# Kernel tuning notes

Measured on AMD Instinct MI355X. Metric: run time of the kernel, lower is better.

## Reference

```python
import jax, jax.numpy as jnp
import numpy as np

B, S, D, H, L, F = 16, 256, 512, 1024, 2, 2048  # batch, seq, inner, head(clusters), layers, ffnn
HID = D // 2
LN_EPS = 1e-5


def _lstm_dir(x, Wih, Whh, bih, bhh, reverse=False):
    # x: [B,S,D] -> hs: [B,S,HID]; PyTorch gate order i,f,g,o
    if reverse:
        x = x[:, ::-1]
    xT = jnp.swapaxes(x, 0, 1)                    # [S,B,D]
    pre = xT @ Wih.T + (bih + bhh)                # precompute input contribution [S,B,4*HID]
    z = jnp.zeros((x.shape[0], Whh.shape[1]), x.dtype)

    def step(carry, p):
        h, c = carry
        g = p + h @ Whh.T
        i, f, gg, o = jnp.split(g, 4, axis=-1)
        c = jax.nn.sigmoid(f) * c + jax.nn.sigmoid(i) * jnp.tanh(gg)
        h = jax.nn.sigmoid(o) * jnp.tanh(c)
        return (h, c), h

    _, hs = jax.lax.scan(step, (z, z), pre)
    hs = jnp.swapaxes(hs, 0, 1)                   # [B,S,HID]
    if reverse:
        hs = hs[:, ::-1]
    return hs


def _layernorm(x, g, b):
    mu = jnp.mean(x, axis=-1, keepdims=True)
    var = jnp.mean(jnp.square(x - mu), axis=-1, keepdims=True)
    return (x - mu) * jax.lax.rsqrt(var + LN_EPS) * g + b


def _forward(input_sequence, label_embeddings, out_proj,
             Wih_f, Whh_f, bih_f, bhh_f, Wih_b, Whh_b, bih_b, bhh_b,
             ffnn_w1, ffnn_b1, ffnn_w2, ffnn_b2, ln_g, ln_b):
    fwd = _lstm_dir(input_sequence, Wih_f, Whh_f, bih_f, bhh_f, reverse=False)
    bwd = _lstm_dir(input_sequence, Wih_b, Whh_b, bih_b, bhh_b, reverse=True)
    features = jnp.concatenate([fwd, bwd], axis=-1)          # [B,S,D]

    query = jnp.broadcast_to(label_embeddings, (input_sequence.shape[0], H, D))
    for l in range(L):
        # self-attention (no scaling, as in source)
        w = jax.nn.softmax(jnp.einsum('bqd,bkd->bqk', query, query), axis=-1)
        q1 = jnp.einsum('bqk,bkd->bqd', w, query)
        # cross-attention onto LSTM features
        w2 = jax.nn.softmax(jnp.einsum('bqd,bsd->bqs', q1, features), axis=-1)
        q2 = jnp.einsum('bqs,bsd->bqd', w2, features)
        # FFN + LayerNorm
        h = jax.nn.gelu(q2 @ ffnn_w1[l] + ffnn_b1[l], approximate=False) @ ffnn_w2[l] + ffnn_b2[l]
        query = _layernorm(h, ln_g[l], ln_b[l])
    # (query @ output) * eye @ ones  ==  diagonal of the matmul == batched dot
    return jnp.einsum('bhd,dh->bh', query, out_proj)


def setup_inputs() -> dict:
    ks = jax.random.split(jax.random.key(0), 20)
    s_lstm = 1.0 / np.sqrt(HID)
    s_ff = 0.02
    clusters = jax.random.normal(ks[0], (H, D), jnp.float32) * s_ff
    return {
        'input_sequence': jax.random.normal(ks[1], (B, S, D), jnp.float32),
        'label_embeddings': clusters,
        'out_proj': clusters.T,
        'Wih_f': jax.random.normal(ks[2], (4 * HID, D), jnp.float32) * s_lstm,
        'Whh_f': jax.random.normal(ks[3], (4 * HID, HID), jnp.float32) * s_lstm,
        'bih_f': jax.random.normal(ks[4], (4 * HID,), jnp.float32) * s_lstm,
        'bhh_f': jax.random.normal(ks[5], (4 * HID,), jnp.float32) * s_lstm,
        'Wih_b': jax.random.normal(ks[6], (4 * HID, D), jnp.float32) * s_lstm,
        'Whh_b': jax.random.normal(ks[7], (4 * HID, HID), jnp.float32) * s_lstm,
        'bih_b': jax.random.normal(ks[8], (4 * HID,), jnp.float32) * s_lstm,
        'bhh_b': jax.random.normal(ks[9], (4 * HID,), jnp.float32) * s_lstm,
        'ffnn_w1': jax.random.normal(ks[10], (L, D, F), jnp.float32) * s_ff,
        'ffnn_b1': jnp.zeros((L, F), jnp.float32),
        'ffnn_w2': jax.random.normal(ks[11], (L, F, D), jnp.float32) * s_ff,
        'ffnn_b2': jnp.zeros((L, D), jnp.float32),
        'ln_g': jnp.ones((L, D), jnp.float32),
        'ln_b': jnp.zeros((L, D), jnp.float32),
    }


def reference(input_sequence, label_embeddings, out_proj,
              Wih_f, Whh_f, bih_f, bhh_f, Wih_b, Whh_b, bih_b, bhh_b,
              ffnn_w1, ffnn_b1, ffnn_w2, ffnn_b2, ln_g, ln_b):
    return _forward(input_sequence, label_embeddings, out_proj,
                    Wih_f, Whh_f, bih_f, bhh_f, Wih_b, Whh_b, bih_b, bhh_b,
                    ffnn_w1, ffnn_b1, ffnn_w2, ffnn_b2, ln_g, ln_b)
```

## Files before the change

kernel.cpp:

```cpp
#include <hip/hip_runtime.h>
#include <hip/hip_bf16.h>
#include <math.h>

#define NB 16
#define NS 256
#define ND 512
#define NH 1024
#define NF 2048
#define NHID 256

typedef __attribute__((ext_vector_type(8))) short bf16x8;
typedef __attribute__((ext_vector_type(4))) float f32x4;

__device__ __forceinline__ unsigned short f2bf(float f) {
    unsigned u = __float_as_uint(f);
    unsigned r = u + 0x7fffu + ((u >> 16) & 1u);
    return (unsigned short)(r >> 16);
}
__device__ __forceinline__ float bf2f(unsigned short h) {
    return __uint_as_float(((unsigned)h) << 16);
}
__device__ __forceinline__ float sigmoid_fast(float x) {
    return 1.0f / (1.0f + __expf(-x));
}
__device__ __forceinline__ float tanh_fast(float x) {
    return 1.0f - 2.0f / (__expf(2.0f * x) + 1.0f);
}

template<int PASSES, int ACT, int OUT>
__global__ __launch_bounds__(256) void sgemm4(
    const unsigned short* __restrict__ Ahi, const unsigned short* __restrict__ Alo,
    const unsigned short* __restrict__ Bhi, const unsigned short* __restrict__ Blo,
    const float* __restrict__ bias,
    float* __restrict__ C, unsigned short* __restrict__ Chi, unsigned short* __restrict__ Clo,
    int M, int N, int K, int lda, int ldb, long sA, long sB, long sC)
{
    __shared__ unsigned short Ah[128 * 32];
    __shared__ unsigned short Bh[128 * 32];
    __shared__ unsigned short Al[(PASSES == 3) ? 128 * 32 : 64];
    __shared__ unsigned short Bl[(PASSES == 3) ? 128 * 32 : 64];

    const int t = threadIdx.x;
    const int z = blockIdx.z;
    const int m0 = blockIdx.y * 128, n0 = blockIdx.x * 128;
    const int wid = t >> 6, lane = t & 63;
    const int wr = (wid >> 1) * 64, wc = (wid & 1) * 64;
    const int lr = lane & 15, lk = lane >> 4;
    const int rl = lane >> 2, sl = lane & 3;

    const unsigned short* pAh = Ahi + (size_t)z * sA;
    const unsigned short* pBh = Bhi + (size_t)z * sB;
    const unsigned short* pAl = (PASSES == 3) ? Alo + (size_t)z * sA : nullptr;
    const unsigned short* pBl = (PASSES == 3) ? Blo + (size_t)z * sB : nullptr;

    f32x4 acc[4][4];
    #pragma unroll
    for (int i = 0; i < 4; ++i)
        #pragma unroll
        for (int j = 0; j < 4; ++j) acc[i][j] = (f32x4){0.f, 0.f, 0.f, 0.f};

    for (int k0 = 0; k0 < K; k0 += 32) {
        #pragma unroll
        for (int e = 0; e < 2; ++e) {
            const int r = e * 64 + wid * 16 + rl;
            const size_t goA = (size_t)(m0 + r) * lda + k0 + sl * 8;
            const size_t goB = (size_t)(n0 + r) * ldb + k0 + sl * 8;
            const int lo = (e * 64 + wid * 16) * 32;
            __builtin_amdgcn_global_load_lds((const void*)(pAh + goA), (void*)&Ah[lo], 16, 0, 0);
            __builtin_amdgcn_global_load_lds((const void*)(pBh + goB), (void*)&Bh[lo], 16, 0, 0);
            if (PASSES == 3) {
                __builtin_amdgcn_global_load_lds((const void*)(pAl + goA), (void*)&Al[lo], 16, 0, 0);
                __builtin_amdgcn_global_load_lds((const void*)(pBl + goB), (void*)&Bl[lo], 16, 0, 0);
            }
        }
        __syncthreads();

        bf16x8 ah[4], bh[4], al[4], bl[4];
        #pragma unroll
        for (int mt = 0; mt < 4; ++mt) {
            int rf = wr + mt * 16 + lr;
            ah[mt] = *(const bf16x8*)&Ah[rf * 32 + lk * 8];
            if (PASSES == 3) al[mt] = *(const bf16x8*)&Al[rf * 32 + lk * 8];
        }
        #pragma unroll
        for (int nt = 0; nt < 4; ++nt) {
            int rf = wc + nt * 16 + lr;
            bh[nt] = *(const bf16x8*)&Bh[rf * 32 + lk * 8];
            if (PASSES == 3) bl[nt] = *(const bf16x8*)&Bl[rf * 32 + lk * 8];
        }
        #pragma unroll
        for (int mt = 0; mt < 4; ++mt)
            #pragma unroll
            for (int nt = 0; nt < 4; ++nt) {
                acc[mt][nt] = __builtin_amdgcn_mfma_f32_16x16x32_bf16(ah[mt], bh[nt], acc[mt][nt], 0, 0, 0);
                if (PASSES == 3) {
                    acc[mt][nt] = __builtin_amdgcn_mfma_f32_16x16x32_bf16(al[mt], bh[nt], acc[mt][nt], 0, 0, 0);
                    acc[mt][nt] = __builtin_amdgcn_mfma_f32_16x16x32_bf16(ah[mt], bl[nt], acc[mt][nt], 0, 0, 0);
                }
            }
        __syncthreads();
    }

    #pragma unroll
    for (int nt = 0; nt < 4; ++nt) {
        int col = n0 + wc + nt * 16 + lr;
        float bv = bias ? bias[col] : 0.0f;
        #pragma unroll
        for (int mt = 0; mt < 4; ++mt) {
            #pragma unroll
            for (int i = 0; i < 4; ++i) {
                int row = m0 + wr + mt * 16 + lk * 4 + i;
                float x = acc[mt][nt][i] + bv;
                if (ACT == 1) x = 0.5f * x * (1.0f + erff(x * 0.70710678118654752f));
                size_t oi = (size_t)z * sC + (size_t)row * N + col;
                if (OUT == 1) {
                    unsigned short h = f2bf(x);
                    Chi[oi] = h;
                    Clo[oi] = f2bf(x - bf2f(h));
                } else if (OUT == 2) {
                    Chi[oi] = f2bf(x);
                } else {
                    C[oi] = x;
                }
            }
        }
    }
}

static void gemm4(int passes, int act, int outm,
                  const unsigned short* Ahi, const unsigned short* Alo,
                  const unsigned short* Bhi, const unsigned short* Blo,
                  const float* bias, float* C, unsigned short* Chi, unsigned short* Clo,
                  int M, int N, int K, int lda, int ldb,
                  long sA, long sB, long sC, int Z, hipStream_t st)
{
    dim3 g(N / 128, M / 128, Z), b(256);
    if (passes == 3) {
        sgemm4<3, 0, 0><<<g, b, 0, st>>>(Ahi, Alo, Bhi, Blo, bias, C, Chi, Clo, M, N, K, lda, ldb, sA, sB, sC);
    } else if (outm == 1) {
        sgemm4<1, 0, 1><<<g, b, 0, st>>>(Ahi, Alo, Bhi, Blo, bias, C, Chi, Clo, M, N, K, lda, ldb, sA, sB, sC);
    } else if (outm == 2 && act == 1) {
        sgemm4<1, 1, 2><<<g, b, 0, st>>>(Ahi, Alo, Bhi, Blo, bias, C, Chi, Clo, M, N, K, lda, ldb, sA, sB, sC);
    } else if (outm == 2) {
        sgemm4<1, 0, 2><<<g, b, 0, st>>>(Ahi, Alo, Bhi, Blo, bias, C, Chi, Clo, M, N, K, lda, ldb, sA, sB, sC);
    } else {
        sgemm4<1, 0, 0><<<g, b, 0, st>>>(Ahi, Alo, Bhi, Blo, bias, C, Chi, Clo, M, N, K, lda, ldb, sA, sB, sC);
    }
}

__global__ __launch_bounds__(256) void ffn2_ln(
    const unsigned short* __restrict__ A, const unsigned short* __restrict__ B,
    const float* __restrict__ bias, const float* __restrict__ g, const float* __restrict__ bb,
    unsigned short* __restrict__ Ohi, unsigned short* __restrict__ Olo)
{
    __shared__ unsigned short Ah[64 * 32];
    __shared__ unsigned short Bh[512 * 32];
    __shared__ float stats[64][4][2];

    const int t = threadIdx.x;
    const int m0 = blockIdx.x * 64;
    const int wid = t >> 6, lane = t & 63;
    const int lr = lane & 15, lk = lane >> 4;
    const int wc = wid * 128;
    const int rl = lane >> 2, sl = lane & 3;

    f32x4 acc[4][8];
    #pragma unroll
    for (int i = 0; i < 4; ++i)
        #pragma unroll
        for (int j = 0; j < 8; ++j) acc[i][j] = (f32x4){0.f, 0.f, 0.f, 0.f};

    for (int k0 = 0; k0 < NF; k0 += 32) {
        __builtin_amdgcn_global_load_lds(
            (const void*)(A + (size_t)(m0 + wid * 16 + rl) * NF + k0 + sl * 8),
            (void*)&Ah[(wid * 16) * 32], 16, 0, 0);
        #pragma unroll
        for (int e = 0; e < 8; ++e) {
            int r = e * 64 + wid * 16 + rl;
            __builtin_amdgcn_global_load_lds(
                (const void*)(B + (size_t)r * NF + k0 + sl * 8),
                (void*)&Bh[(e * 64 + wid * 16) * 32], 16, 0, 0);
        }
        __syncthreads();

        bf16x8 af[4], bf[8];
        #pragma unroll
        for (int mt = 0; mt < 4; ++mt)
            af[mt] = *(const bf16x8*)&Ah[(mt * 16 + lr) * 32 + lk * 8];
        #pragma unroll
        for (int nt = 0; nt < 8; ++nt)
            bf[nt] = *(const bf16x8*)&Bh[(wc + nt * 16 + lr) * 32 + lk * 8];
        #pragma unroll
        for (int mt = 0; mt < 4; ++mt)
            #pragma unroll
            for (int nt = 0; nt < 8; ++nt)
                acc[mt][nt] = __builtin_amdgcn_mfma_f32_16x16x32_bf16(af[mt], bf[nt], acc[mt][nt], 0, 0, 0);
        __syncthreads();
    }

    float bv[8];
    #pragma unroll
    for (int nt = 0; nt < 8; ++nt) bv[nt] = bias[wc + nt * 16 + lr];

    float psum[4][4], psq[4][4];
    #pragma unroll
    for (int mt = 0; mt < 4; ++mt)
        #pragma unroll
        for (int i = 0; i < 4; ++i) {
            float s = 0.f, q = 0.f;
            #pragma unroll
            for (int nt = 0; nt < 8; ++nt) {
                float x = acc[mt][nt][i] + bv[nt];
                acc[mt][nt][i] = x;
                s += x;
                q += x * x;
            }
            psum[mt][i] = s;
            psq[mt][i] = q;
        }
    #pragma unroll
    for (int o = 1; o <= 8; o <<= 1)
        #pragma unroll
        for (int mt = 0; mt < 4; ++mt)
            #pragma unroll
            for (int i = 0; i < 4; ++i) {
                psum[mt][i] += __shfl_xor(psum[mt][i], o);
                psq[mt][i]  += __shfl_xor(psq[mt][i], o);
            }
    if (lr == 0) {
        #pragma unroll
        for (int mt = 0; mt < 4; ++mt)
            #pragma unroll
            for (int i = 0; i < 4; ++i) {
                int r = mt * 16 + lk * 4 + i;
                stats[r][wid][0] = psum[mt][i];
                stats[r][wid][1] = psq[mt][i];
            }
    }
    __syncthreads();

    float gv[8], betav[8];
    #pragma unroll
    for (int nt = 0; nt < 8; ++nt) {
        gv[nt]    = g[wc + nt * 16 + lr];
        betav[nt] = bb[wc + nt * 16 + lr];
    }
    #pragma unroll
    for (int mt = 0; mt < 4; ++mt)
        #pragma unroll
        for (int i = 0; i < 4; ++i) {
            int r = mt * 16 + lk * 4 + i;
            float s = stats[r][0][0] + stats[r][1][0] + stats[r][2][0] + stats[r][3][0];
            float q = stats[r][0][1] + stats[r][1][1] + stats[r][2][1] + stats[r][3][1];
            float mu = s * (1.0f / 512.0f);
            float var = q * (1.0f / 512.0f) - mu * mu;
            float inv = rsqrtf(var + 1e-5f);
            #pragma unroll
            for (int nt = 0; nt < 8; ++nt) {
                float y = (acc[mt][nt][i] - mu) * inv * gv[nt] + betav[nt];
                size_t oi = (size_t)(m0 + r) * 512 + wc + nt * 16 + lr;
                unsigned short h = f2bf(y);
                Ohi[oi] = h;
                Olo[oi] = f2bf(y - bf2f(h));
            }
        }
}

__global__ __launch_bounds__(256) void cvt_split(const float* __restrict__ in,
                                                 unsigned short* __restrict__ hi,
                                                 unsigned short* __restrict__ lo)
{
    size_t i = ((size_t)blockIdx.x * 256 + threadIdx.x) * 4;
    float4 v = *(const float4*)(in + i);
    ushort4 h, l;
    h.x = f2bf(v.x); l.x = f2bf(v.x - bf2f(h.x));
    h.y = f2bf(v.y); l.y = f2bf(v.y - bf2f(h.y));
    h.z = f2bf(v.z); l.z = f2bf(v.z - bf2f(h.z));
    h.w = f2bf(v.w); l.w = f2bf(v.w - bf2f(h.w));
    *(ushort4*)(hi + i) = h;
    *(ushort4*)(lo + i) = l;
}

__global__ __launch_bounds__(256) void cvt_split_t(const float* __restrict__ in,
                                                   unsigned short* __restrict__ hiT,
                                                   unsigned short* __restrict__ loT,
                                                   int R, int C)
{
    __shared__ unsigned short tileH[64 * 72];
    __shared__ unsigned short tileL[64 * 72];
    int r0 = blockIdx.y * 64, c0 = blockIdx.x * 64;
    int t = threadIdx.x;
    int tr = t >> 2, tc = (t & 3) * 16;

    float v[16];
    const float* src = in + (size_t)(r0 + tr) * C + c0 + tc;
    *(float4*)(v)      = *(const float4*)(src);
    *(float4*)(v + 4)  = *(const float4*)(src + 4);
    *(float4*)(v + 8)  = *(const float4*)(src + 8);
    *(float4*)(v + 12) = *(const float4*)(src + 12);
    #pragma unroll
    for (int i = 0; i < 16; ++i) {
        unsigned short h = f2bf(v[i]);
        tileH[(tc + i) * 72 + tr] = h;
        tileL[(tc + i) * 72 + tr] = f2bf(v[i] - bf2f(h));
    }
    __syncthreads();

    size_t ob = (size_t)(c0 + tr) * R + r0 + tc;
    *(uint4*)(hiT + ob)     = *(const uint4*)(&tileH[tr * 72 + tc]);
    *(uint4*)(hiT + ob + 8) = *(const uint4*)(&tileH[tr * 72 + tc + 8]);
    *(uint4*)(loT + ob)     = *(const uint4*)(&tileL[tr * 72 + tc]);
    *(uint4*)(loT + ob + 8) = *(const uint4*)(&tileL[tr * 72 + tc + 8]);
}

__global__ __launch_bounds__(256) void tcvt_bf16(const unsigned short* __restrict__ in,
                                                 unsigned short* __restrict__ out,
                                                 int R, int C)
{
    __shared__ unsigned short tile[64 * 72];
    int z = blockIdx.z;
    in += (size_t)z * R * C;
    out += (size_t)z * R * C;
    int r0 = blockIdx.y * 64, c0 = blockIdx.x * 64;
    int t = threadIdx.x;
    int tr = t >> 2, tc = (t & 3) * 16;

    uint4 q0 = *(const uint4*)(in + (size_t)(r0 + tr) * C + c0 + tc);
    uint4 q1 = *(const uint4*)(in + (size_t)(r0 + tr) * C + c0 + tc + 8);
    unsigned short e[16];
    *(uint4*)(e) = q0;
    *(uint4*)(e + 8) = q1;
    #pragma unroll
    for (int i = 0; i < 16; ++i) tile[(tc + i) * 72 + tr] = e[i];
    __syncthreads();

    uint4 o0 = *(const uint4*)(&tile[tr * 72 + tc]);
    uint4 o1 = *(const uint4*)(&tile[tr * 72 + tc + 8]);
    *(uint4*)(out + (size_t)(c0 + tr) * R + r0 + tc) = o0;
    *(uint4*)(out + (size_t)(c0 + tr) * R + r0 + tc + 8) = o1;
}

__global__ __launch_bounds__(256) void bias_sum_kernel(
    const float* bihF, const float* bhhF, const float* bihB, const float* bhhB,
    float* out)
{
    int i = blockIdx.x * 256 + threadIdx.x;
    if (i < 1024) out[i] = bihF[i] + bhhF[i];
    else out[i] = bihB[i - 1024] + bhhB[i - 1024];
}

__global__ __launch_bounds__(256) void rec_fused(
    const float* __restrict__ pre,
    const float* __restrict__ WhhF, const float* __restrict__ WhhB,
    unsigned long long* __restrict__ hg, int* __restrict__ flags,
    unsigned short* __restrict__ fhi, unsigned short* __restrict__ flo,
    const unsigned short* __restrict__ lehi, const unsigned short* __restrict__ lelo,
    float* __restrict__ wsc,
    const float* __restrict__ w1, const float* __restrict__ w2,
    unsigned short* __restrict__ w1th0, unsigned short* __restrict__ w2th0,
    unsigned short* __restrict__ w1th1, unsigned short* __restrict__ w2th1,
    const float* __restrict__ proj,
    unsigned short* __restrict__ pth, unsigned short* __restrict__ ptl)
{
    __shared__ unsigned short hh[16 * 264];
    __shared__ unsigned short hl[16 * 264];
    __shared__ float gx[4][16][17];
    __shared__ unsigned short gAh[128 * 32];
    __shared__ unsigned short gAl[128 * 32];
    __shared__ unsigned short gBh[128 * 32];
    __shared__ unsigned short gBl[128 * 32];
    __shared__ unsigned short tH[64 * 72];
    __shared__ unsigned short tL[64 * 72];

    const int tid = threadIdx.x;

    if (blockIdx.x < 32) {
        const int bid = blockIdx.x;
        const int dir = bid >> 4, slice = bid & 15;
        const float* Whh = dir ? WhhB : WhhF;
        const int wv = tid >> 6;
        const int lane = tid & 63;
        const int lr = lane & 15;
        const int lk = lane >> 4;
        const int eb = tid >> 4;
        const int eu = tid & 15;

        bf16x8 wfh[8], wfl[8];
        {
            const float* wrow = Whh + (size_t)(wv * 256 + slice * 16 + lr) * 256 + lk * 8;
            #pragma unroll
            for (int kt = 0; kt < 8; ++kt) {
                float4 a = *(const float4*)(wrow + kt * 32);
                float4 b = *(const float4*)(wrow + kt * 32 + 4);
                float v[8] = {a.x, a.y, a.z, a.w, b.x, b.y, b.z, b.w};
                unsigned short hhv[8], llv[8];
                #pragma unroll
                for (int i = 0; i < 8; ++i) {
                    unsigned short h = f2bf(v[i]);
                    hhv[i] = h;
                    llv[i] = f2bf(v[i] - bf2f(h));
                }
                wfh[kt] = *(bf16x8*)hhv;
                wfl[kt] = *(bf16x8*)llv;
            }
        }
        for (int i = tid; i < 16 * 264; i += 256) { hh[i] = 0; hl[i] = 0; }

        float c = 0.0f;
        __syncthreads();

        for (int si = 0; si < NS; ++si) {
            const int s = dir ? (NS - 1 - si) : si;
            const float* pp = pre + ((size_t)(eb * NS + s)) * 2048 + dir * 1024 + slice * 16 + eu;
            float pi = pp[0], pf = pp[256], pg = pp[512], po = pp[768];

            if (si > 0) {
                if (tid < 16) {
                    while (__hip_atomic_load(&flags[dir * 16 + tid], __ATOMIC_RELAXED,
                                             __HIP_MEMORY_SCOPE_AGENT) < si) {
                        __builtin_amdgcn_s_sleep(1);
                    }
                }
                __syncthreads();
                const unsigned long long* src =
                    hg + (size_t)(((si - 1) & 1) * 2 + dir) * 2048;
                const int b2 = tid >> 4, pb = (tid & 15) * 8;
                unsigned short hbuf[16], lbuf[16];
                #pragma unroll
                for (int j = 0; j < 8; ++j) {
                    unsigned long long v = __hip_atomic_load(
                        &src[b2 * 128 + pb + j], __ATOMIC_RELAXED,
                        __HIP_MEMORY_SCOPE_AGENT);
                    hbuf[2 * j]     = (unsigned short)(v & 0xffff);
                    lbuf[2 * j]     = (unsigned short)((v >> 16) & 0xffff);
                    hbuf[2 * j + 1] = (unsigned short)((v >> 32) & 0xffff);
                    lbuf[2 * j + 1] = (unsigned short)(v >> 48);
                }
                char* dh = (char*)hh + b2 * 528 + (tid & 15) * 32;
                char* dl = (char*)hl + b2 * 528 + (tid & 15) * 32;
                *(uint4*)dh        = *(uint4*)(hbuf);
                *(uint4*)(dh + 16) = *(uint4*)(hbuf + 8);
                *(uint4*)dl        = *(uint4*)(lbuf);
                *(uint4*)(dl + 16) = *(uint4*)(lbuf + 8);
                __syncthreads();
            }

            f32x4 acc = (f32x4){0.f, 0.f, 0.f, 0.f};
            #pragma unroll
            for (int kt = 0; kt < 8; ++kt) {
                const char* hp = (const char*)hh + lr * 528 + kt * 64 + lk * 16;
                const char* lp = (const char*)hl + lr * 528 + kt * 64 + lk * 16;
                bf16x8 ah = *(const bf16x8*)hp;
                bf16x8 al = *(const bf16x8*)lp;
                acc = __builtin_amdgcn_mfma_f32_16x16x32_bf16(ah, wfh[kt], acc, 0, 0, 0);
                acc = __builtin_amdgcn_mfma_f32_16x16x32_bf16(al, wfh[kt], acc, 0, 0, 0);
                acc = __builtin_amdgcn_mfma_f32_16x16x32_bf16(ah, wfl[kt], acc, 0, 0, 0);
            }
            #pragma unroll
            for (int i = 0; i < 4; ++i) gx[wv][lk * 4 + i][lr] = acc[i];
            __syncthreads();

            float ai = gx[0][eb][eu] + pi;
            float af = gx[1][eb][eu] + pf;
            float ag = gx[2][eb][eu] + pg;
            float ao = gx[3][eb][eu] + po;
            float gi = sigmoid_fast(ai);
            float gf = sigmoid_fast(af);
            float gg = tanh_fast(ag);
            float go = sigmoid_fast(ao);
            c = gf * c + gi * gg;
            float h = go * tanh_fast(c);

            unsigned short h16 = f2bf(h);
            unsigned short l16 = f2bf(h - bf2f(h16));
            unsigned my = (unsigned)h16 | ((unsigned)l16 << 16);
            unsigned oth = __shfl_xor(my, 1);
            if ((eu & 1) == 0) {
                unsigned long long v = (unsigned long long)my |
                                       ((unsigned long long)oth << 32);
                unsigned long long* dst =
                    hg + (size_t)((si & 1) * 2 + dir) * 2048;
                __hip_atomic_store(&dst[eb * 128 + slice * 8 + (eu >> 1)], v,
                                   __ATOMIC_RELAXED, __HIP_MEMORY_SCOPE_AGENT);
            }
            size_t oi = ((size_t)(eb * NS + s)) * 512 + dir * 256 + slice * 16 + eu;
            fhi[oi] = h16;
            flo[oi] = l16;

            asm volatile("s_waitcnt vmcnt(0)" ::: "memory");
            __syncthreads();
            if (tid == 0)
                __hip_atomic_store(&flags[bid], si + 1, __ATOMIC_RELAXED,
                                   __HIP_MEMORY_SCOPE_AGENT);
        }
        return;
    }

    const int hid = blockIdx.x - 32;
    const int lane = tid & 63;
    const int wid = tid >> 6;
    const int lr = lane & 15, lk = lane >> 4;

    if (hid < 64) {
        const int m0 = (hid >> 3) * 128, n0 = (hid & 7) * 128;
        const int wr = (wid >> 1) * 64, wc = (wid & 1) * 64;
        const int sr = tid >> 1, sc = (tid & 1) * 16;

        f32x4 acc[4][4];
        #pragma unroll
        for (int i = 0; i < 4; ++i)
            #pragma unroll
            for (int j = 0; j < 4; ++j) acc[i][j] = (f32x4){0.f, 0.f, 0.f, 0.f};

        for (int k0 = 0; k0 < ND; k0 += 32) {
            {
                size_t oa = (size_t)(m0 + sr) * ND + k0 + sc;
                size_t ob = (size_t)(n0 + sr) * ND + k0 + sc;
                *(uint4*)&gAh[sr * 32 + sc]     = *(const uint4*)(lehi + oa);
                *(uint4*)&gAh[sr * 32 + sc + 8] = *(const uint4*)(lehi + oa + 8);
                *(uint4*)&gAl[sr * 32 + sc]     = *(const uint4*)(lelo + oa);
                *(uint4*)&gAl[sr * 32 + sc + 8] = *(const uint4*)(lelo + oa + 8);
                *(uint4*)&gBh[sr * 32 + sc]     = *(const uint4*)(lehi + ob);
                *(uint4*)&gBh[sr * 32 + sc + 8] = *(const uint4*)(lehi + ob + 8);
                *(uint4*)&gBl[sr * 32 + sc]     = *(const uint4*)(lelo + ob);
                *(uint4*)&gBl[sr * 32 + sc + 8] = *(const uint4*)(lelo + ob + 8);
            }
            __syncthreads();

            bf16x8 ah[4], al[4], bh[4], bl[4];
            #pragma unroll
            for (int mt = 0; mt < 4; ++mt) {
                int rf = wr + mt * 16 + lr;
                ah[mt] = *(const bf16x8*)&gAh[rf * 32 + lk * 8];
                al[mt] = *(const bf16x8*)&gAl[rf * 32 + lk * 8];
            }
            #pragma unroll
            for (int nt = 0; nt < 4; ++nt) {
                int rf = wc + nt * 16 + lr;
                bh[nt] = *(const bf16x8*)&gBh[rf * 32 + lk * 8];
                bl[nt] = *(const bf16x8*)&gBl[rf * 32 + lk * 8];
            }
            #pragma unroll
            for (int mt = 0; mt < 4; ++mt)
                #pragma unroll
                for (int nt = 0; nt < 4; ++nt) {
                    acc[mt][nt] = __builtin_amdgcn_mfma_f32_16x16x32_bf16(ah[mt], bh[nt], acc[mt][nt], 0, 0, 0);
                    acc[mt][nt] = __builtin_amdgcn_mfma_f32_16x16x32_bf16(al[mt], bh[nt], acc[mt][nt], 0, 0, 0);
                    acc[mt][nt] = __builtin_amdgcn_mfma_f32_16x16x32_bf16(ah[mt], bl[nt], acc[mt][nt], 0, 0, 0);
                }
            __syncthreads();
        }
        const int wr2 = (wid >> 1) * 64, wc2 = (wid & 1) * 64;
        #pragma unroll
        for (int nt = 0; nt < 4; ++nt) {
            int col = n0 + wc2 + nt * 16 + lr;
            #pragma unroll
            for (int mt = 0; mt < 4; ++mt)
                #pragma unroll
                for (int i = 0; i < 4; ++i) {
                    int row = m0 + wr2 + mt * 16 + lk * 4 + i;
                    wsc[(size_t)row * NH + col] = acc[mt][nt][i];
                }
        }
    }

    const int tr = tid >> 2, tc = (tid & 3) * 16;
    for (int job = hid; job < 1152; job += 224) {
        const float* in;
        unsigned short* outH;
        unsigned short* outL = nullptr;
        int R, C, by, bx;
        if (job < 256)        { int j = job;        in = w1;              outH = w1th0; R = ND; C = NF; by = j >> 5, bx = j & 31; }
        else if (job < 512)   { int j = job - 256;  in = w2;              outH = w2th0; R = NF; C = ND; by = j >> 3, bx = j & 7; }
        else if (job < 768)   { int j = job - 512;  in = w1 + (size_t)ND * NF; outH = w1th1; R = ND; C = NF; by = j >> 5, bx = j & 31; }
        else if (job < 1024)  { int j = job - 768;  in = w2 + (size_t)NF * ND; outH = w2th1; R = NF; C = ND; by = j >> 3, bx = j & 7; }
        else                  { int j = job - 1024; in = proj;            outH = pth; outL = ptl; R = 512; C = 1024; by = j >> 4, bx = j & 15; }

        int r0 = by * 64, c0 = bx * 64;
        __syncthreads();
        float v[16];
        const float* src = in + (size_t)(r0 + tr) * C + c0 + tc;
        *(float4*)(v)      = *(const float4*)(src);
        *(float4*)(v + 4)  = *(const float4*)(src + 4);
        *(float4*)(v + 8)  = *(const float4*)(src + 8);
        *(float4*)(v + 12) = *(const float4*)(src + 12);
        if (outL) {
            #pragma unroll
            for (int i = 0; i < 16; ++i) {
                unsigned short h = f2bf(v[i]);
                tH[(tc + i) * 72 + tr] = h;
                tL[(tc + i) * 72 + tr] = f2bf(v[i] - bf2f(h));
            }
        } else {
            #pragma unroll
            for (int i = 0; i < 16; ++i) tH[(tc + i) * 72 + tr] = f2bf(v[i]);
        }
        __syncthreads();
        size_t ob = (size_t)(c0 + tr) * R + r0 + tc;
        *(uint4*)(outH + ob)     = *(const uint4*)(&tH[tr * 72 + tc]);
        *(uint4*)(outH + ob + 8) = *(const uint4*)(&tH[tr * 72 + tc + 8]);
        if (outL) {
            *(uint4*)(outL + ob)     = *(const uint4*)(&tL[tr * 72 + tc]);
            *(uint4*)(outL + ob + 8) = *(const uint4*)(&tL[tr * 72 + tc + 8]);
        }
    }
}

__global__ __launch_bounds__(256) void post_rec(
    const unsigned short* __restrict__ fhi, const unsigned short* __restrict__ flo,
    unsigned short* __restrict__ fthi, unsigned short* __restrict__ ftlo,
    float* __restrict__ wsc)
{
    __shared__ unsigned short tile[64 * 72];
    __shared__ float lm[4];
    __shared__ float ls[4];
    const int t = threadIdx.x;

    if (blockIdx.x < 1024) {
        int job = blockIdx.x;
        const unsigned short* in;
        unsigned short* out;
        if (job < 512) { in = fhi; out = fthi; } else { in = flo; out = ftlo; job -= 512; }
        const int R = 256, C = 512;
        int z = job >> 5, jj = job & 31;
        int bx = jj & 7, by = jj >> 3;
        in  += (size_t)z * R * C;
        out += (size_t)z * R * C;
        int r0 = by * 64, c0 = bx * 64;
        int tr = t >> 2, tc = (t & 3) * 16;

        uint4 q0 = *(const uint4*)(in + (size_t)(r0 + tr) * C + c0 + tc);
        uint4 q1 = *(const uint4*)(in + (size_t)(r0 + tr) * C + c0 + tc + 8);
        unsigned short e[16];
        *(uint4*)(e) = q0;
        *(uint4*)(e + 8) = q1;
        #pragma unroll
        for (int i = 0; i < 16; ++i) tile[(tc + i) * 72 + tr] = e[i];
        __syncthreads();

        *(uint4*)(out + (size_t)(c0 + tr) * R + r0 + tc)     = *(const uint4*)(&tile[tr * 72 + tc]);
        *(uint4*)(out + (size_t)(c0 + tr) * R + r0 + tc + 8) = *(const uint4*)(&tile[tr * 72 + tc + 8]);
        return;
    }

    const int N = 1024;
    float* row = wsc + (size_t)(blockIdx.x - 1024) * N;
    unsigned short* o = (unsigned short*)row;
    float v[4];
    float m = -1e30f;
    #pragma unroll
    for (int i = 0; i < 4; ++i) { v[i] = row[t + (i << 8)]; m = fmaxf(m, v[i]); }
    for (int sh = 32; sh; sh >>= 1) m = fmaxf(m, __shfl_xor(m, sh));
    if ((t & 63) == 0) lm[t >> 6] = m;
    __syncthreads();
    m = fmaxf(fmaxf(lm[0], lm[1]), fmaxf(lm[2], lm[3]));
    float s = 0.0f;
    #pragma unroll
    for (int i = 0; i < 4; ++i) { v[i] = expf(v[i] - m); s += v[i]; }
    for (int sh = 32; sh; sh >>= 1) s += __shfl_xor(s, sh);
    if ((t & 63) == 0) ls[t >> 6] = s;
    __syncthreads();
    s = ls[0] + ls[1] + ls[2] + ls[3];
    float inv = 1.0f / s;
    __syncthreads();
    #pragma unroll
    for (int i = 0; i < 4; ++i) {
        float y = v[i] * inv;
        unsigned short h = f2bf(y);
        int j = t + (i << 8);
        o[j] = h;
        o[N + j] = f2bf(y - bf2f(h));
    }
}

__global__ __launch_bounds__(256) void softmax_ip(float* __restrict__ X, int N)
{
    float* row = X + (size_t)blockIdx.x * N;
    unsigned short* o = (unsigned short*)row;
    int t = threadIdx.x;
    int cnt = N >> 8;
    float v[4];
    float m = -1e30f;
    for (int i = 0; i < cnt; ++i) { v[i] = row[t + (i << 8)]; m = fmaxf(m, v[i]); }
    for (int sh = 32; sh; sh >>= 1) m = fmaxf(m, __shfl_xor(m, sh));
    __shared__ float lm[4];
    if ((t & 63) == 0) lm[t >> 6] = m;
    __syncthreads();
    m = fmaxf(fmaxf(lm[0], lm[1]), fmaxf(lm[2], lm[3]));
    float s = 0.0f;
    for (int i = 0; i < cnt; ++i) { v[i] = expf(v[i] - m); s += v[i]; }
    for (int sh = 32; sh; sh >>= 1) s += __shfl_xor(s, sh);
    __shared__ float ls[4];
    if ((t & 63) == 0) ls[t >> 6] = s;
    __syncthreads();
    s = ls[0] + ls[1] + ls[2] + ls[3];
    float inv = 1.0f / s;
    __syncthreads();
    for (int i = 0; i < cnt; ++i) {
        float y = v[i] * inv;
        unsigned short h = f2bf(y);
        int j = t + (i << 8);
        o[j] = h;
        o[N + j] = f2bf(y - bf2f(h));
    }
}

__global__ __launch_bounds__(256) void outproj3(
    const unsigned short* __restrict__ qhi, const unsigned short* __restrict__ qlo,
    const unsigned short* __restrict__ phi, const unsigned short* __restrict__ plo,
    float* __restrict__ out)
{
    int gw = blockIdx.x * 4 + (threadIdx.x >> 6);
    int lane = threadIdx.x & 63;
    int h = gw & 1023;
    uint4 qh = ((const uint4*)(qhi + (size_t)gw * 512))[lane];
    uint4 ql = ((const uint4*)(qlo + (size_t)gw * 512))[lane];
    uint4 ph = ((const uint4*)(phi + (size_t)h * 512))[lane];
    uint4 pl = ((const uint4*)(plo + (size_t)h * 512))[lane];
    unsigned short qhe[8], qle[8], phe[8], ple[8];
    *(uint4*)qhe = qh; *(uint4*)qle = ql; *(uint4*)phe = ph; *(uint4*)ple = pl;
    float s = 0.0f;
    #pragma unroll
    for (int i = 0; i < 8; ++i) {
        float q = bf2f(qhe[i]) + bf2f(qle[i]);
        float p = bf2f(phe[i]) + bf2f(ple[i]);
        s += q * p;
    }
    for (int o = 32; o; o >>= 1) s += __shfl_xor(s, o);
    if (lane == 0) out[gw] = s;
}

extern "C" void kernel_launch(void* const* d_in, const int* in_sizes, int n_in,
                              void* d_out, int out_size, void* d_ws, size_t ws_size,
                              hipStream_t stream)
{
    (void)in_sizes; (void)n_in; (void)out_size; (void)ws_size;

    const float* x     = (const float*)d_in[0];
    const float* le    = (const float*)d_in[1];
    const float* proj  = (const float*)d_in[2];
    const float* WihF  = (const float*)d_in[3];
    const float* WhhF  = (const float*)d_in[4];
    const float* bihF  = (const float*)d_in[5];
    const float* bhhF  = (const float*)d_in[6];
    const float* WihB  = (const float*)d_in[7];
    const float* WhhB  = (const float*)d_in[8];
    const float* bihB  = (const float*)d_in[9];
    const float* bhhB  = (const float*)d_in[10];
    const float* w1    = (const float*)d_in[11];
    const float* b1    = (const float*)d_in[12];
    const float* w2    = (const float*)d_in[13];
    const float* b2    = (const float*)d_in[14];
    const float* lng   = (const float*)d_in[15];
    const float* lnb   = (const float*)d_in[16];
    float* out = (float*)d_out;
    float* ws  = (float*)d_ws;
    unsigned short* wsu = (unsigned short*)d_ws;

    const size_t MEG = 1048576;
    const size_t R0    = 0;
    const size_t R1    = 8 * MEG;
    const size_t AR    = 16 * MEG;
    const size_t QHI   = 33 * MEG;
    const size_t QLO   = 37 * MEG;
    const size_t FHI   = 41 * MEG;
    const size_t FLO   = 42 * MEG;
    const size_t FTHI  = 43 * MEG;
    const size_t FTLO  = 44 * MEG;
    const size_t LEHI  = 45 * MEG;
    const size_t LELO  = LEHI  + MEG / 4;
    const size_t LETHI = LELO  + MEG / 4;
    const size_t LETLO = LETHI + MEG / 4;
    const size_t WIHH  = 46 * MEG;
    const size_t WIHL  = WIHH + MEG / 2;
    const size_t SYNC  = 47 * MEG;
    const size_t W1TH0 = SYNC  + MEG / 4;
    const size_t W1TH1 = W1TH0 + MEG / 2;
    const size_t W2TH0 = W1TH1 + MEG / 2;
    const size_t W2TH1 = W2TH0 + MEG / 2;
    const size_t PTH   = W2TH1 + MEG / 2;
    const size_t PTL   = PTH   + MEG / 4;
    const size_t BSUM  = PTL   + MEG / 4;

    float* pre    = ws + R0;
    float* arena  = ws + AR;
    float* bsum   = ws + BSUM;
    int*   flags  = (int*)(ws + SYNC);
    unsigned long long* hg = (unsigned long long*)(ws + SYNC + 1024);
    unsigned short* qthi  = wsu + 2 * R0;
    unsigned short* q2hi  = wsu + 2 * R1;
    unsigned short* qhi   = wsu + 2 * QHI;
    unsigned short* qlo   = wsu + 2 * QLO;
    unsigned short* fhi   = wsu + 2 * FHI;
    unsigned short* flo   = wsu + 2 * FLO;
    unsigned short* fthi  = wsu + 2 * FTHI;
    unsigned short* ftlo  = wsu + 2 * FTLO;
    unsigned short* lehi  = wsu + 2 * LEHI;
    unsigned short* lelo  = wsu + 2 * LELO;
    unsigned short* lethi = wsu + 2 * LETHI;
    unsigned short* letlo = wsu + 2 * LETLO;
    unsigned short* wihh  = wsu + 2 * WIHH;
    unsigned short* wihl  = wsu + 2 * WIHL;
    unsigned short* w1th0 = wsu + 2 * W1TH0;
    unsigned short* w1th1 = wsu + 2 * W1TH1;
    unsigned short* w2th0 = wsu + 2 * W2TH0;
    unsigned short* w2th1 = wsu + 2 * W2TH1;
    unsigned short* pth   = wsu + 2 * PTH;
    unsigned short* ptl   = wsu + 2 * PTL;

    bias_sum_kernel<<<8, 256, 0, stream>>>(bihF, bhhF, bihB, bhhB, bsum);
    cvt_split<<<512, 256, 0, stream>>>(WihF, wihh, wihl);
    cvt_split<<<512, 256, 0, stream>>>(WihB, wihh + 524288, wihl + 524288);
    cvt_split<<<512, 256, 0, stream>>>(le, lehi, lelo);
    { dim3 g(512 / 64, 1024 / 64, 1);
      cvt_split_t<<<g, 256, 0, stream>>>(le, lethi, letlo, 1024, 512); }
    hipMemsetAsync(flags, 0, 32 * sizeof(int), stream);

    unsigned short* xhi = wsu + 2 * AR;
    unsigned short* xlo = wsu + 2 * (AR + MEG);
    cvt_split<<<2048, 256, 0, stream>>>(x, xhi, xlo);

    gemm4(3, 0, 0, xhi, xlo, wihh, wihl, bsum, pre, nullptr, nullptr,
          NB * NS, 2048, ND, ND, ND, 0, 0, 0, 1, stream);

    float* wsc_l0 = arena;
    rec_fused<<<256, 256, 0, stream>>>(pre, WhhF, WhhB, hg, flags, fhi, flo,
                                       lehi, lelo, wsc_l0,
                                       w1, w2, w1th0, w2th0, w1th1, w2th1,
                                       proj, pth, ptl);

    post_rec<<<2048, 256, 0, stream>>>(fhi, flo, fthi, ftlo, wsc_l0);

    for (int l = 0; l < 2; ++l) {
        const float* b1l = b1 + (size_t)l * NF;
        const float* b2l = b2 + (size_t)l * ND;
        const float* gl  = lng + (size_t)l * ND;
        const float* bl  = lnb + (size_t)l * ND;
        unsigned short* w1th = l ? w1th1 : w1th0;
        unsigned short* w2th = l ? w2th1 : w2th0;

        if (l == 0) {
            unsigned short* wscu = (unsigned short*)wsc_l0;
            unsigned short* q1hi = wsu + 2 * (AR + 1 * MEG);
            unsigned short* q1lo = wsu + 2 * (AR + 1 * MEG + MEG / 4);
            float* s2s = arena + 4 * MEG;
            unsigned short* s2u = (unsigned short*)s2s;

            gemm4(1, 0, 1, wscu, nullptr, lethi, nullptr, nullptr, nullptr, q1hi, q1lo,
                  NH, ND, NH, 2 * NH, NH, 0, 0, 0, 1, stream);
            gemm4(3, 0, 0, q1hi, q1lo, fhi, flo, nullptr, s2s, nullptr, nullptr,
                  NH, NS, ND, ND, ND, 0, (long)NS * ND, (long)NH * NS, 16, stream);
            softmax_ip<<<NB * NH, 256, 0, stream>>>(s2s, NS);
            gemm4(1, 0, 2, s2u, nullptr, fthi, nullptr, nullptr, nullptr, q2hi, nullptr,
                  NH, ND, NS, 2 * NS, NS,
                  (long)2 * NH * NS, (long)ND * NS, (long)NH * ND, 16, stream);
        } else {
            { dim3 g(512 / 64, 1024 / 64, 16);
              tcvt_bf16<<<g, 256, 0, stream>>>(qhi, qthi, 1024, 512); }
            float* wsc = arena;
            unsigned short* wscu = (unsigned short*)wsc;
            unsigned short* q1hi = wsu + 2 * (AR + 8 * MEG);
            unsigned short* q1lo = wsu + 2 * (AR + 10 * MEG);
            float* s2s = arena + 12 * MEG;
            unsigned short* s2u = (unsigned short*)s2s;
            for (int g8 = 0; g8 < 2; ++g8) {
                size_t qo = (size_t)g8 * 8;
                gemm4(3, 0, 0, qhi + qo * NH * ND, qlo + qo * NH * ND,
                      qhi + qo * NH * ND, qlo + qo * NH * ND, nullptr, wsc, nullptr, nullptr,
                      NH, NH, ND, ND, ND,
                      (long)NH * ND, (long)NH * ND, (long)NH * NH, 8, stream);
                softmax_ip<<<8 * NH, 256, 0, stream>>>(wsc, NH);
                gemm4(1, 0, 1, wscu, nullptr, qthi + qo * ND * NH, nullptr,
                      nullptr, nullptr, q1hi, q1lo, NH, ND, NH, 2 * NH, NH,
                      (long)2 * NH * NH, (long)ND * NH, (long)NH * ND, 8, stream);
                gemm4(3, 0, 0, q1hi, q1lo, fhi + qo * NS * ND, flo + qo * NS * ND,
                      nullptr, s2s, nullptr, nullptr, NH, NS, ND, ND, ND,
                      (long)NH * ND, (long)NS * ND, (long)NH * NS, 8, stream);
                softmax_ip<<<8 * NH, 256, 0, stream>>>(s2s, NS);
                gemm4(1, 0, 2, s2u, nullptr, fthi + qo * ND * NS, nullptr,
                      nullptr, nullptr, q2hi + qo * NH * ND, nullptr,
                      NH, ND, NS, 2 * NS, NS,
                      (long)2 * NH * NS, (long)ND * NS, (long)NH * ND, 8, stream);
            }
        }

        unsigned short* ffhi = wsu + 2 * AR;
        gemm4(1, 1, 2, q2hi, nullptr, w1th, nullptr, b1l, nullptr, ffhi, nullptr,
              16384, NF, ND, ND, ND, 0, 0, 0, 1, stream);
        ffn2_ln<<<256, 256, 0, stream>>>(ffhi, w2th, b2l, gl, bl, qhi, qlo);
    }

    outproj3<<<4096, 256, 0, stream>>>(qhi, qlo, pth, ptl, out);
}
```

Before: 1.502 ms.

## Exploit symmetry of Q·Qᵀ scores and batch all sixteen attention heads at once

Adds a dedicated 3-pass bf16 split GEMM for the self-attention score matrix Q·Qᵀ. It computes only the upper-triangular 128x128 tiles (36 of 64) and mirrors each result into the transposed position, which cuts the score-GEMM MFMA work nearly in half. It also drops the two-pass loop over groups of 8 batches and launches each stage once over all 16 batches, with workspace buffers moved to fit the larger batch. The mirrored writes are strided, transposed stores that may be poorly coalesced, and the new buffer placement must not alias live data.

```diff
diff --git a/kernel.cpp b/kernel.cpp
--- a/kernel.cpp
+++ b/kernel.cpp
@@ -145,6 +145,94 @@
         sgemm4<1, 0, 2><<<g, b, 0, st>>>(Ahi, Alo, Bhi, Blo, bias, C, Chi, Clo, M, N, K, lda, ldb, sA, sB, sC);
     } else {
         sgemm4<1, 0, 0><<<g, b, 0, st>>>(Ahi, Alo, Bhi, Blo, bias, C, Chi, Clo, M, N, K, lda, ldb, sA, sB, sC);
+    }
+}
+
+__global__ __launch_bounds__(256) void sgemm_sym3(
+    const unsigned short* __restrict__ Qhi, const unsigned short* __restrict__ Qlo,
+    float* __restrict__ C, long sA, long sC)
+{
+    __shared__ unsigned short Ah[128 * 32];
+    __shared__ unsigned short Bh[128 * 32];
+    __shared__ unsigned short Al[128 * 32];
+    __shared__ unsigned short Bl[128 * 32];
+
+    const int t = threadIdx.x;
+    const int z = blockIdx.z;
+    int tt = blockIdx.x, by = 0;
+    #pragma unroll
+    for (int r = 0; r < 8; ++r) {
+        if (tt >= r + 1 && by == r) { tt -= r + 1; by = r + 1; }
+    }
+    const int bx = tt;
+    const int m0 = by * 128, n0 = bx * 128;
+
+    const int wid = t >> 6, lane = t & 63;
+    const int wr = (wid >> 1) * 64, wc = (wid & 1) * 64;
+    const int lr = lane & 15, lk = lane >> 4;
+    const int rl = lane >> 2, sl = lane & 3;
+
+    const unsigned short* pAh = Qhi + (size_t)z * sA;
+    const unsigned short* pAl = Qlo + (size_t)z * sA;
+
+    f32x4 acc[4][4];
+    #pragma unroll
+    for (int i = 0; i < 4; ++i)
+        #pragma unroll
+        for (int j = 0; j < 4; ++j) acc[i][j] = (f32x4){0.f, 0.f, 0.f, 0.f};
+
+    for (int k0 = 0; k0 < ND; k0 += 32) {
+        #pragma unroll
+        for (int e = 0; e < 2; ++e) {
+            const int r = e * 64 + wid * 16 + rl;
+            const size_t goA = (size_t)(m0 + r) * ND + k0 + sl * 8;
+            const size_t goB = (size_t)(n0 + r) * ND + k0 + sl * 8;
+            const int lo = (e * 64 + wid * 16) * 32;
+            __builtin_amdgcn_global_load_lds((const void*)(pAh + goA), (void*)&Ah[lo], 16, 0, 0);
+            __builtin_amdgcn_global_load_lds((const void*)(pAh + goB), (void*)&Bh[lo], 16, 0, 0);
+            __builtin_amdgcn_global_load_lds((const void*)(pAl + goA), (void*)&Al[lo], 16, 0, 0);
+            __builtin_amdgcn_global_load_lds((const void*)(pAl + goB), (void*)&Bl[lo], 16, 0, 0);
+        }
+        __syncthreads();
+
+        bf16x8 ah[4], bh[4], al[4], bl[4];
+        #pragma unroll
+        for (int mt = 0; mt < 4; ++mt) {
+            int rf = wr + mt * 16 + lr;
+            ah[mt] = *(const bf16x8*)&Ah[rf * 32 + lk * 8];
+            al[mt] = *(const bf16x8*)&Al[rf * 32 + lk * 8];
+        }
+        #pragma unroll
+        for (int nt = 0; nt < 4; ++nt) {
+            int rf = wc + nt * 16 + lr;
+            bh[nt] = *(const bf16x8*)&Bh[rf * 32 + lk * 8];
+            bl[nt] = *(const bf16x8*)&Bl[rf * 32 + lk * 8];
+        }
+        #pragma unroll
+        for (int mt = 0; mt < 4; ++mt)
+            #pragma unroll
+            for (int nt = 0; nt < 4; ++nt) {
+                acc[mt][nt] = __builtin_amdgcn_mfma_f32_16x16x32_bf16(ah[mt], bh[nt], acc[mt][nt], 0, 0, 0);
+                acc[mt][nt] = __builtin_amdgcn_mfma_f32_16x16x32_bf16(al[mt], bh[nt], acc[mt][nt], 0, 0, 0);
+                acc[mt][nt] = __builtin_amdgcn_mfma_f32_16x16x32_bf16(ah[mt], bl[nt], acc[mt][nt], 0, 0, 0);
+            }
+        __syncthreads();
+    }
+
+    float* Cz = C + (size_t)z * sC;
+    #pragma unroll
+    for (int nt = 0; nt < 4; ++nt) {
+        int col = n0 + wc + nt * 16 + lr;
+        #pragma unroll
+        for (int mt = 0; mt < 4; ++mt) {
+            #pragma unroll
+            for (int i = 0; i < 4; ++i) {
+                int row = m0 + wr + mt * 16 + lk * 4 + i;
+                float x = acc[mt][nt][i];
+                Cz[(size_t)row * NH + col] = x;
+                if (by != bx) Cz[(size_t)col * NH + row] = x;
+            }
+        }
     }
 }
 
@@ -859,29 +947,25 @@
               tcvt_bf16<<<g, 256, 0, stream>>>(qhi, qthi, 1024, 512); }
             float* wsc = arena;
             unsigned short* wscu = (unsigned short*)wsc;
-            unsigned short* q1hi = wsu + 2 * (AR + 8 * MEG);
-            unsigned short* q1lo = wsu + 2 * (AR + 10 * MEG);
-            float* s2s = arena + 12 * MEG;
+            unsigned short* q1hi = wsu + 2 * (R0 + 4 * MEG);
+            unsigned short* q1lo = wsu + 2 * (R1 + 4 * MEG);
+            float* s2s = ws + QLO;
             unsigned short* s2u = (unsigned short*)s2s;
-            for (int g8 = 0; g8 < 2; ++g8) {
-                size_t qo = (size_t)g8 * 8;
-                gemm4(3, 0, 0, qhi + qo * NH * ND, qlo + qo * NH * ND,
-                      qhi + qo * NH * ND, qlo + qo * NH * ND, nullptr, wsc, nullptr, nullptr,
-                      NH, NH, ND, ND, ND,
-                      (long)NH * ND, (long)NH * ND, (long)NH * NH, 8, stream);
-                softmax_ip<<<8 * NH, 256, 0, stream>>>(wsc, NH);
-                gemm4(1, 0, 1, wscu, nullptr, qthi + qo * ND * NH, nullptr,
-                      nullptr, nullptr, q1hi, q1lo, NH, ND, NH, 2 * NH, NH,
-                      (long)2 * NH * NH, (long)ND * NH, (long)NH * ND, 8, stream);
-                gemm4(3, 0, 0, q1hi, q1lo, fhi + qo * NS * ND, flo + qo * NS * ND,
-                      nullptr, s2s, nullptr, nullptr, NH, NS, ND, ND, ND,
-                      (long)NH * ND, (long)NS * ND, (long)NH * NS, 8, stream);
-                softmax_ip<<<8 * NH, 256, 0, stream>>>(s2s, NS);
-                gemm4(1, 0, 2, s2u, nullptr, fthi + qo * ND * NS, nullptr,
-                      nullptr, nullptr, q2hi + qo * NH * ND, nullptr,
-                      NH, ND, NS, 2 * NS, NS,
-                      (long)2 * NH * NS, (long)ND * NS, (long)NH * ND, 8, stream);
-            }
+
+            { dim3 g(36, 1, 16), b(256);
+              sgemm_sym3<<<g, b, 0, stream>>>(qhi, qlo, wsc,
+                                              (long)NH * ND, (long)NH * NH); }
+            softmax_ip<<<16 * NH, 256, 0, stream>>>(wsc, NH);
+            gemm4(1, 0, 1, wscu, nullptr, qthi, nullptr, nullptr, nullptr, q1hi, q1lo,
+                  NH, ND, NH, 2 * NH, NH,
+                  (long)2 * NH * NH, (long)ND * NH, (long)NH * ND, 16, stream);
+            gemm4(3, 0, 0, q1hi, q1lo, fhi, flo, nullptr, s2s, nullptr, nullptr,
+                  NH, NS, ND, ND, ND,
+                  (long)NH * ND, (long)NS * ND, (long)NH * NS, 16, stream);
+            softmax_ip<<<16 * NH, 256, 0, stream>>>(s2s, NS);
+            gemm4(1, 0, 2, s2u, nullptr, fthi, nullptr, nullptr, nullptr, q2hi, nullptr,
+                  NH, ND, NS, 2 * NS, NS,
+                  (long)2 * NH * NS, (long)ND * NS, (long)NH * ND, 16, stream);
         }
 
         unsigned short* ffhi = wsu + 2 * AR;
```

Measured after the change: 1.489 ms. About the same (-0.9%).
